# Kernel tuning notes

Measured on AMD Instinct MI355X. Metric: run time of the kernel, lower is better.

## Reference

```python
import jax, jax.numpy as jnp
import numpy as np

B, T, HOR, N = 64, 12, 12, 1024
DIN, DOUT, YCOV, H, K, E = 1, 1, 1, 64, 3, 8


def setup_inputs() -> dict:
    key = jax.random.key(0)
    ks = jax.random.split(key, 10)
    def g(k, shape, s=1.0):
        return jax.random.normal(k, shape, dtype=jnp.float32) * s
    # xavier-ish scale for GCN weights: 1/sqrt(fan_in)
    gi = 1.0 / np.sqrt(K * (DIN + H))
    di = 1.0 / np.sqrt(K * (DOUT + YCOV + H))
    return {
        "x": jax.random.uniform(ks[0], (B, T, N, DIN), dtype=jnp.float32),
        "y_cov": jax.random.uniform(ks[1], (B, HOR, N, YCOV), dtype=jnp.float32),
        "node_emb": g(ks[2], (N, E), 1.0),
        "enc_gate_W": g(ks[3], (K * (DIN + H), 2 * H), gi),
        "enc_gate_b": jnp.zeros((2 * H,), jnp.float32),
        "enc_upd_W": g(ks[4], (K * (DIN + H), H), gi),
        "enc_upd_b": jnp.zeros((H,), jnp.float32),
        "dec_gate_W": g(ks[5], (K * (DOUT + YCOV + H), 2 * H), di),
        "dec_gate_b": jnp.zeros((2 * H,), jnp.float32),
        "dec_upd_W": g(ks[6], (K * (DOUT + YCOV + H), H), di),
        "dec_upd_b": jnp.zeros((H,), jnp.float32),
        "proj_W": g(ks[7], (H, DOUT), 1.0 / np.sqrt(H)),
        "proj_b": jnp.zeros((DOUT,), jnp.float32),
    }


def _cheb_supports(A):
    # support_set = [I, A, 2*A@A - I, ...], cheb_k terms
    s = [jnp.eye(A.shape[0], dtype=A.dtype), A]
    for _ in range(2, K):
        s.append(2.0 * A @ s[-1] - s[-2])
    return jnp.stack(s)  # [K, N, N]


def _gcn(x, sup, W, b):
    # x: [B,N,C]; sup: [K,N,N]; matches torch cat([s_k @ x], -1) ordering (k-major)
    bb, nn, cc = x.shape
    xg = jnp.einsum('knm,bmc->bnkc', sup, x).reshape(bb, nn, K * cc)
    return xg @ W + b


def _cell(x, h, sup, gW, gb, uW, ub):
    zr = jax.nn.sigmoid(_gcn(jnp.concatenate([x, h], -1), sup, gW, gb))
    z, r = jnp.split(zr, 2, axis=-1)
    hc = jnp.tanh(_gcn(jnp.concatenate([x, z * h], -1), sup, uW, ub))
    return r * h + (1.0 - r) * hc


def reference(x, y_cov, node_emb, enc_gate_W, enc_gate_b, enc_upd_W, enc_upd_b,
              dec_gate_W, dec_gate_b, dec_upd_W, dec_upd_b, proj_W, proj_b):
    # adaptive adjacency from node embeddings (AGCRN-style)
    A = jax.nn.softmax(jax.nn.relu(node_emb @ node_emb.T), axis=-1)
    sup = _cheb_supports(A)

    h0 = jnp.zeros((B, N, H), x.dtype)

    def enc_step(h, xt):
        h2 = _cell(xt, h, sup, enc_gate_W, enc_gate_b, enc_upd_W, enc_upd_b)
        return h2, None
    h_enc, _ = jax.lax.scan(enc_step, h0, jnp.swapaxes(x, 0, 1))  # final state [B,N,H]

    go0 = jnp.zeros((B, N, DOUT), x.dtype)

    def dec_step(carry, yt):
        h, go = carry
        h2 = _cell(jnp.concatenate([go, yt], -1), h, sup,
                   dec_gate_W, dec_gate_b, dec_upd_W, dec_upd_b)
        go2 = h2 @ proj_W + proj_b
        return (h2, go2), go2
    _, outs = jax.lax.scan(dec_step, (h_enc, go0), jnp.swapaxes(y_cov, 0, 1))
    return jnp.swapaxes(outs, 0, 1)  # [B, HOR, N, DOUT]
```

## Files before the change

kernel.cpp:

```cpp
#include <hip/hip_runtime.h>
#include <math.h>

constexpr int N = 1024, B = 64, T = 12, HOR = 12, H = 64, E = 8;
constexpr size_t NBH = 4194304;

constexpr size_t A_off   = 0;
constexpr size_t Pxy_off = 1048576;
constexpr size_t h_off   = Pxy_off + 3145728;
constexpr size_t Ph_off  = h_off + NBH;
constexpr size_t zh_off  = Ph_off + 2 * NBH;
constexpr size_t r_off   = zh_off + NBH;
constexpr size_t go_off  = r_off + NBH;
constexpr size_t A2_off  = go_off + 65536;
constexpr size_t Bth_off = A2_off + 1048576;
constexpr size_t Btz_off = Bth_off + 2162688;
constexpr size_t xyK_off = Btz_off + 2097152;
constexpr size_t Pgo_off = xyK_off + 786432;
constexpr size_t wp_off  = Pgo_off + 131072;

typedef __attribute__((ext_vector_type(8))) short short8;
typedef _Float16 half8 __attribute__((ext_vector_type(8)));
typedef __attribute__((ext_vector_type(4))) float f32x4;

__device__ __forceinline__ unsigned f2bf(float x) {
  unsigned u = __float_as_uint(x);
  return (u + 0x7fffu + ((u >> 16) & 1u)) >> 16;
}
__device__ __forceinline__ float bf2f(unsigned h) {
  return __uint_as_float(h << 16);
}
__device__ __forceinline__ ushort f2h(float x) {
  _Float16 h = (_Float16)x;
  ushort u;
  __builtin_memcpy(&u, &h, 2);
  return u;
}
__device__ __forceinline__ void split4(float4 v, uint2& hi, uint2& lo) {
  unsigned h0 = f2bf(v.x), h1 = f2bf(v.y), h2 = f2bf(v.z), h3 = f2bf(v.w);
  unsigned l0 = f2bf(v.x - bf2f(h0)), l1 = f2bf(v.y - bf2f(h1));
  unsigned l2 = f2bf(v.z - bf2f(h2)), l3 = f2bf(v.w - bf2f(h3));
  hi.x = (h0 & 0xffffu) | (h1 << 16); hi.y = (h2 & 0xffffu) | (h3 << 16);
  lo.x = (l0 & 0xffffu) | (l1 << 16); lo.y = (l2 & 0xffffu) | (l3 << 16);
}

typedef const __attribute__((address_space(1))) void gas_t;
typedef __attribute__((address_space(3))) void las_t;

__global__ __launch_bounds__(256) void build_A(const float* __restrict__ emb,
                                               float* __restrict__ A) {
  __shared__ float sE[N * E];
  __shared__ float sv[N];
  __shared__ float rmax[4], rsum[4];
  const int i = blockIdx.x;
  for (int idx = threadIdx.x; idx < N * E / 4; idx += 256)
    ((float4*)sE)[idx] = ((const float4*)emb)[idx];
  __syncthreads();
  float ei[E];
#pragma unroll
  for (int e = 0; e < E; ++e) ei[e] = sE[i * E + e];
  float mymax = 0.f;
  for (int j = threadIdx.x; j < N; j += 256) {
    float d = 0.f;
#pragma unroll
    for (int e = 0; e < E; ++e) d = fmaf(ei[e], sE[j * E + e], d);
    d = fmaxf(d, 0.f);
    sv[j] = d;
    mymax = fmaxf(mymax, d);
  }
  for (int off = 32; off; off >>= 1) mymax = fmaxf(mymax, __shfl_down(mymax, off));
  const int wid = threadIdx.x >> 6, lid = threadIdx.x & 63;
  if (lid == 0) rmax[wid] = mymax;
  __syncthreads();
  const float m = fmaxf(fmaxf(rmax[0], rmax[1]), fmaxf(rmax[2], rmax[3]));
  float mysum = 0.f;
  for (int j = threadIdx.x; j < N; j += 256) {
    float ev = expf(sv[j] - m);
    sv[j] = ev;
    mysum += ev;
  }
  for (int off = 32; off; off >>= 1) mysum += __shfl_down(mysum, off);
  if (lid == 0) rsum[wid] = mysum;
  __syncthreads();
  const float inv = 1.f / (rsum[0] + rsum[1] + rsum[2] + rsum[3]);
  for (int j = threadIdx.x; j < N; j += 256) A[i * N + j] = sv[j] * inv;
}

__global__ __launch_bounds__(256) void pack_split_S(const float* __restrict__ A,
                                                    ushort* __restrict__ L,
                                                    ushort* __restrict__ R) {
  __shared__ float tile[32][33];
  const int bx = blockIdx.x * 32;
  const int by = blockIdx.y * 32;
  const int tx = threadIdx.x & 31;
  const int tg = threadIdx.x >> 5;
#pragma unroll
  for (int p = 0; p < 4; ++p) {
    int ty = tg * 4 + p;
    tile[ty][tx] = A[(size_t)(by + ty) * 1024 + bx + tx];
  }
  __syncthreads();
#pragma unroll
  for (int p = 0; p < 4; ++p) {
    int ty = tg * 4 + p;
    float v = tile[ty][tx];
    unsigned h = f2bf(v);
    unsigned l = f2bf(v - bf2f(h));
    size_t lb = (size_t)(by + ty) * 3072 + 3 * (bx + tx);
    L[lb + 0] = (ushort)h; L[lb + 1] = (ushort)l; L[lb + 2] = (ushort)h;
    float w = tile[tx][ty];
    unsigned hh = f2bf(w);
    unsigned ll = f2bf(w - bf2f(hh));
    size_t rbi = (size_t)(bx + ty) * 3072 + 3 * (by + tx);
    R[rbi + 0] = (ushort)hh; R[rbi + 1] = (ushort)hh; R[rbi + 2] = (ushort)ll;
  }
}

__global__ __launch_bounds__(256) void conv_bf16(const float* __restrict__ src,
                                                 ushort* __restrict__ dst) {
  int i = blockIdx.x * 256 + threadIdx.x;
  float4 v = ((const float4*)src)[i];
  ushort4 o;
  o.x = (ushort)f2bf(v.x); o.y = (ushort)f2bf(v.y);
  o.z = (ushort)f2bf(v.z); o.w = (ushort)f2bf(v.w);
  ((ushort4*)dst)[i] = o;
}

__global__ __launch_bounds__(256) void conv_xyK(const float* __restrict__ src,
                                                ushort* __restrict__ dst, int off) {
  int id = blockIdx.x * 256 + threadIdx.x;
  int tb = id >> 10, n = id & 1023;
  int tt = tb >> 6, b = tb & 63;
  dst[(size_t)(off + tb) * 1024 + n] = (ushort)f2bf(src[((size_t)b * T + tt) * 1024 + n]);
}

__global__ __launch_bounds__(256) void pack_Wbf(const float* __restrict__ W,
                                                ushort* __restrict__ out,
                                                int CIN, int NC, int xoff) {
  int idx = blockIdx.x * 256 + threadIdx.x;
  int total = 2 * NC * 32;
  if (idx >= total) return;
  int kk = idx & 31;
  int rest = idx >> 5;
  int col = rest % NC;
  int half = rest / NC;
  float v = W[(size_t)(xoff + half * 32 + kk) * NC + col];
  unsigned hi = f2bf(v);
  unsigned lo = f2bf(v - bf2f(hi));
  size_t base = (size_t)(half * 2) * NC * 32;
  out[base + (size_t)col * 32 + kk] = (ushort)hi;
  out[base + (size_t)NC * 32 + (size_t)col * 32 + kk] = (ushort)lo;
}

__global__ __launch_bounds__(256) void pack_W16(const float* __restrict__ W,
                                                ushort* __restrict__ out,
                                                int CIN, int NC, int xoff) {
  int idx = blockIdx.x * 256 + threadIdx.x;
  int total = 2 * 2 * NC * 32;
  if (idx >= total) return;
  int kk = idx & 31;
  int rest = idx >> 5;
  int col = rest % NC;
  rest /= NC;
  int half = rest & 1;
  int s1 = rest >> 1;
  int s = s1 + 1;
  float v = W[(size_t)(s * CIN + xoff + half * 32 + kk) * NC + col];
  out[(size_t)(s1 * 2 + half) * NC * 32 + (size_t)col * 32 + kk] = f2h(v);
}

__global__ __launch_bounds__(256) void gemm_s2p(
    const ushort* __restrict__ L, const ushort* __restrict__ R,
    float* __restrict__ P) {
  __shared__ ushort As[128 * 32];
  __shared__ ushort Bs[128 * 32];
  const int t = threadIdx.x;
  const int wave = t >> 6, lane = t & 63;
  const int bm = blockIdx.y * 128, bn = blockIdx.x * 128;
  const int wm = (wave & 1) * 64, wn = (wave >> 1) * 64;
  float* Pz = P + (size_t)blockIdx.z * 1048576;
  const int kbase = blockIdx.z * 768;

  const ushort* aSrc[2]; const ushort* bSrc[2];
  ushort* aDst[2]; ushort* bDst[2];
#pragma unroll
  for (int u = 0; u < 2; ++u) {
    int idx = wave * 128 + u * 64 + lane;
    int row = idx >> 2;
    int kq = (idx & 3) * 8;
    aSrc[u] = L + (size_t)(bm + row) * 3072 + kq;
    bSrc[u] = R + (size_t)(bn + row) * 3072 + kq;
    aDst[u] = &As[(wave * 128 + u * 64) * 8];
    bDst[u] = &Bs[(wave * 128 + u * 64) * 8];
  }
  const int lr = lane & 15;
  const int lk = (lane >> 4) * 8;
  f32x4 acc[4][4];
#pragma unroll
  for (int i = 0; i < 4; ++i)
#pragma unroll
    for (int j = 0; j < 4; ++j) acc[i][j] = {0.f, 0.f, 0.f, 0.f};

  for (int k0 = kbase; k0 < kbase + 768; k0 += 32) {
#pragma unroll
    for (int u = 0; u < 2; ++u) {
      __builtin_amdgcn_global_load_lds((gas_t*)(aSrc[u] + k0), (las_t*)aDst[u], 16, 0, 0);
      __builtin_amdgcn_global_load_lds((gas_t*)(bSrc[u] + k0), (las_t*)bDst[u], 16, 0, 0);
    }
    __syncthreads();
    short8 a[4], b[4];
#pragma unroll
    for (int i = 0; i < 4; ++i) a[i] = *(const short8*)&As[(wm + i * 16 + lr) * 32 + lk];
#pragma unroll
    for (int j = 0; j < 4; ++j) b[j] = *(const short8*)&Bs[(wn + j * 16 + lr) * 32 + lk];
#pragma unroll
    for (int i = 0; i < 4; ++i)
#pragma unroll
      for (int j = 0; j < 4; ++j)
        acc[i][j] = __builtin_amdgcn_mfma_f32_16x16x32_bf16(a[i], b[j], acc[i][j], 0, 0, 0);
    __syncthreads();
  }
  const int cr = (lane >> 4) * 4;
  const int cc = lane & 15;
#pragma unroll
  for (int i = 0; i < 4; ++i)
#pragma unroll
    for (int j = 0; j < 4; ++j) {
      int gm = bm + wm + i * 16 + cr;
      int gn = bn + wn + j * 16 + cc;
#pragma unroll
      for (int r = 0; r < 4; ++r)
        Pz[(size_t)(gm + r) * 1024 + gn] = acc[i][j][r];
    }
}

__global__ __launch_bounds__(256) void comb_s2(const float* __restrict__ P,
                                               ushort* __restrict__ A2) {
  int idx = blockIdx.x * 256 + threadIdx.x;
  float4 a = ((const float4*)P)[idx];
  float4 b = ((const float4*)(P + 1048576))[idx];
  float4 c = ((const float4*)(P + 2097152))[idx];
  float4 d = ((const float4*)(P + 3145728))[idx];
  int base = idx << 2;
  int m = base >> 10, c0 = base & 1023;
  float v0 = 2.f * (a.x + b.x + c.x + d.x) - (m == c0 + 0 ? 1.f : 0.f);
  float v1 = 2.f * (a.y + b.y + c.y + d.y) - (m == c0 + 1 ? 1.f : 0.f);
  float v2 = 2.f * (a.z + b.z + c.z + d.z) - (m == c0 + 2 ? 1.f : 0.f);
  float v3 = 2.f * (a.w + b.w + c.w + d.w) - (m == c0 + 3 ? 1.f : 0.f);
  ushort4 o;
  o.x = (ushort)f2bf(v0); o.y = (ushort)f2bf(v1);
  o.z = (ushort)f2bf(v2); o.w = (ushort)f2bf(v3);
  ((ushort4*)(A2 + 1048576))[idx] = o;
}

template <int CMODE>
__global__ __launch_bounds__(256) void gemm_bt(
    const ushort* __restrict__ A2, const ushort* __restrict__ Bt, int n1,
    ushort* __restrict__ C1h, float* __restrict__ C1f, float* __restrict__ C2) {
  __shared__ ushort As[2][128 * 32];
  __shared__ ushort Bs[2][128 * 32];
  const int t = threadIdx.x;
  const int wave = t >> 6, lane = t & 63;
  int bxi, byi;
  if (CMODE == 0) {
    bxi = blockIdx.x; byi = blockIdx.y;
  } else {
    int lin = blockIdx.x;
    if (lin < 512) {
      bxi = (lin & 7) * 4 + ((lin >> 3) & 3);
      byi = lin >> 5;
    } else {
      bxi = 32; byi = lin - 512;
    }
  }
  const int bm = byi * 128, bn = bxi * 128;
  const int wm = (wave & 1) * 64, wn = (wave >> 1) * 64;

  const ushort* aSrc[2]; const ushort* bSrc[2];
  ushort* aDst[2][2]; ushort* bDst[2][2];
#pragma unroll
  for (int u = 0; u < 2; ++u) {
    int idx = wave * 128 + u * 64 + lane;
    int row = idx >> 2;
    int kq = (idx & 3) * 8;
    aSrc[u] = A2 + (size_t)(bm + row) * 1024 + kq;
    bSrc[u] = Bt + (size_t)(bn + row) * 1024 + kq;
#pragma unroll
    for (int p = 0; p < 2; ++p) {
      aDst[p][u] = &As[p][(wave * 128 + u * 64) * 8];
      bDst[p][u] = &Bs[p][(wave * 128 + u * 64) * 8];
    }
  }
  const int lr = lane & 15, lk = (lane >> 4) * 8;
  int aOff[4], bOff[4];
#pragma unroll
  for (int i = 0; i < 4; ++i) {
    aOff[i] = (wm + i * 16 + lr) * 32 + lk;
    bOff[i] = (wn + i * 16 + lr) * 32 + lk;
  }
  f32x4 acc[4][4];
#pragma unroll
  for (int i = 0; i < 4; ++i)
#pragma unroll
    for (int j = 0; j < 4; ++j) acc[i][j] = {0.f, 0.f, 0.f, 0.f};

  for (int k0 = 0; k0 < 1024; k0 += 64) {
#pragma unroll
    for (int p = 0; p < 2; ++p)
#pragma unroll
      for (int u = 0; u < 2; ++u) {
        __builtin_amdgcn_global_load_lds((gas_t*)(aSrc[u] + k0 + p * 32),
                                         (las_t*)aDst[p][u], 16, 0, 0);
        __builtin_amdgcn_global_load_lds((gas_t*)(bSrc[u] + k0 + p * 32),
                                         (las_t*)bDst[p][u], 16, 0, 0);
      }
    __syncthreads();
#pragma unroll
    for (int p = 0; p < 2; ++p) {
      short8 a[4], b[4];
#pragma unroll
      for (int i = 0; i < 4; ++i) a[i] = *(const short8*)&As[p][aOff[i]];
#pragma unroll
      for (int j = 0; j < 4; ++j) b[j] = *(const short8*)&Bs[p][bOff[j]];
#pragma unroll
      for (int i = 0; i < 4; ++i)
#pragma unroll
        for (int j = 0; j < 4; ++j)
          acc[i][j] = __builtin_amdgcn_mfma_f32_16x16x32_bf16(a[i], b[j], acc[i][j], 0, 0, 0);
    }
    __syncthreads();
  }

  const int cr = (lane >> 4) * 4;
  const int cc = lane & 15;
#pragma unroll
  for (int i = 0; i < 4; ++i) {
#pragma unroll
    for (int j = 0; j < 4; ++j) {
      int gm = bm + wm + i * 16 + cr;
      int gn = bn + wn + j * 16 + cc;
      if (gn < n1) {
        if (CMODE == 0) {
          float* p = C1f + (size_t)gm * n1 + gn;
#pragma unroll
          for (int r = 0; r < 4; ++r) p[(size_t)r * n1] = acc[i][j][r];
        } else {
          int half = gm >> 10, nn = gm & 1023;
          ushort* p = C1h + (size_t)half * NBH +
                      ((size_t)(gn >> 6) * 1024 + nn) * 64 + (gn & 63);
#pragma unroll
          for (int r = 0; r < 4; ++r) p[(size_t)r * 64] = f2h(acc[i][j][r]);
        }
      } else if (C2 != nullptr && gn < n1 + 64) {
        float* p = C2 + (size_t)gm * 64 + (gn - n1);
#pragma unroll
        for (int r = 0; r < 4; ++r) p[(size_t)r * 64] = acc[i][j][r];
      }
    }
  }
}

template <int NX>
__global__ __launch_bounds__(256, 4) void gate_mfma(
    const float* __restrict__ hmat, const ushort* __restrict__ Ph16,
    const ushort* __restrict__ Wbf, const ushort* __restrict__ W16,
    const float* __restrict__ Wf, const float* __restrict__ bias,
    const float* __restrict__ xb0, int xbs0, const float* __restrict__ xp0, int xs0,
    const float* __restrict__ xb1, int xbs1, const float* __restrict__ xp1, int xs1,
    float* __restrict__ zh, float* __restrict__ rbuf, ushort* __restrict__ Btz) {
  constexpr int CIN = NX + 64;
  __shared__ ushort smem[12288];
  ushort* Ah = smem;
  ushort* Al = smem + 2048;
  ushort* Bh = smem + 4096;
  ushort* Bl = smem + 8192;
  ushort* A16 = smem;
  ushort* B16 = smem + 4096;
  ushort* transT = smem;
  __shared__ float sxv[3][2][64];
  __shared__ float sWx[3][2][128];
  const int t = threadIdx.x;
  const int wave = t >> 6, lane = t & 63;
  const int bm = blockIdx.x * 64;
  const int wm = (wave & 1) * 32, wn = (wave >> 1) * 64;
  const int lr = lane & 15, lk = (lane >> 4) * 8;

  if (t < 64) {
    int grow = bm + t;
    int n = grow & 1023, b = grow >> 10;
    sxv[0][0][t] = xb0[(size_t)b * xbs0 + n];
    sxv[1][0][t] = xp0[(size_t)n * xs0 + b];
    sxv[2][0][t] = xp0[(size_t)1024 * xs0 + (size_t)n * xs0 + b];
    if (NX == 2) {
      sxv[0][1][t] = xb1[(size_t)b * xbs1 + n];
      sxv[1][1][t] = xp1[(size_t)n * xs1 + b];
      sxv[2][1][t] = xp1[(size_t)1024 * xs1 + (size_t)n * xs1 + b];
    }
  } else if (t < 192) {
    int col = t - 64;
#pragma unroll
    for (int s = 0; s < 3; ++s)
#pragma unroll
      for (int f = 0; f < NX; ++f)
        sWx[s][f][col] = Wf[(size_t)(s * CIN + f) * 128 + col];
  }

  int arow[2], ajq[2];
#pragma unroll
  for (int p = 0; p < 2; ++p) {
    int f = p * 256 + t;
    arow[p] = f >> 3;
    ajq[p] = (f & 7) * 4;
  }
  const int hrow = t >> 2, hjq = (t & 3) * 8;

  float4 pf[2];
#pragma unroll
  for (int p = 0; p < 2; ++p)
    pf[p] = *(const float4*)(hmat + (size_t)(bm + arow[p]) * 64 + ajq[p]);
  uint4 px;

  f32x4 acc[2][4];
#pragma unroll
  for (int i = 0; i < 2; ++i)
#pragma unroll
    for (int j = 0; j < 4; ++j) acc[i][j] = {0.f, 0.f, 0.f, 0.f};

#pragma unroll
  for (int half = 0; half < 2; ++half) {
#pragma unroll
    for (int p = 0; p < 2; ++p) {
      uint2 hi, lo;
      split4(pf[p], hi, lo);
      *(uint2*)&Ah[arow[p] * 32 + ajq[p]] = hi;
      *(uint2*)&Al[arow[p] * 32 + ajq[p]] = lo;
    }
    const ushort* wph = Wbf + (size_t)(half * 2) * (128 * 32);
    const ushort* wpl = wph + 128 * 32;
#pragma unroll
    for (int u = 0; u < 2; ++u) {
      int idx = wave * 128 + u * 64 + lane;
      __builtin_amdgcn_global_load_lds((gas_t*)(wph + idx * 8), (las_t*)&Bh[idx * 8], 16, 0, 0);
      __builtin_amdgcn_global_load_lds((gas_t*)(wpl + idx * 8), (las_t*)&Bl[idx * 8], 16, 0, 0);
    }
    __syncthreads();
    if (half == 0) {
#pragma unroll
      for (int p = 0; p < 2; ++p)
        pf[p] = *(const float4*)(hmat + (size_t)(bm + arow[p]) * 64 + 32 + ajq[p]);
    } else {
      px = *(const uint4*)(Ph16 + (size_t)(bm + hrow) * 64 + hjq);
    }
    short8 ah[2], al[2], bh[4], bl[4];
#pragma unroll
    for (int i = 0; i < 2; ++i) {
      ah[i] = *(const short8*)&Ah[(wm + i * 16 + lr) * 32 + lk];
      al[i] = *(const short8*)&Al[(wm + i * 16 + lr) * 32 + lk];
    }
#pragma unroll
    for (int j = 0; j < 4; ++j) {
      bh[j] = *(const short8*)&Bh[(wn + j * 16 + lr) * 32 + lk];
      bl[j] = *(const short8*)&Bl[(wn + j * 16 + lr) * 32 + lk];
    }
#pragma unroll
    for (int i = 0; i < 2; ++i)
#pragma unroll
      for (int j = 0; j < 4; ++j) {
        acc[i][j] = __builtin_amdgcn_mfma_f32_16x16x32_bf16(ah[i], bh[j], acc[i][j], 0, 0, 0);
        acc[i][j] = __builtin_amdgcn_mfma_f32_16x16x32_bf16(al[i], bh[j], acc[i][j], 0, 0, 0);
        acc[i][j] = __builtin_amdgcn_mfma_f32_16x16x32_bf16(ah[i], bl[j], acc[i][j], 0, 0, 0);
      }
    __syncthreads();
  }

  for (int it = 0; it < 4; ++it) {
    const int s1 = it >> 1, half = it & 1;
    *(uint4*)&A16[hrow * 32 + hjq] = px;
    const ushort* w16 = W16 + (size_t)(s1 * 2 + half) * (128 * 32);
#pragma unroll
    for (int u = 0; u < 2; ++u) {
      int idx = wave * 128 + u * 64 + lane;
      __builtin_amdgcn_global_load_lds((gas_t*)(w16 + idx * 8), (las_t*)&B16[idx * 8], 16, 0, 0);
    }
    __syncthreads();
    if (it < 3) {
      const int nit = it + 1;
      const ushort* src = Ph16 + (size_t)(nit >> 1) * NBH;
      px = *(const uint4*)(src + (size_t)(bm + hrow) * 64 + (nit & 1) * 32 + hjq);
    }
    half8 a16[2], b16[4];
#pragma unroll
    for (int i = 0; i < 2; ++i)
      a16[i] = *(const half8*)&A16[(wm + i * 16 + lr) * 32 + lk];
#pragma unroll
    for (int j = 0; j < 4; ++j)
      b16[j] = *(const half8*)&B16[(wn + j * 16 + lr) * 32 + lk];
#pragma unroll
    for (int i = 0; i < 2; ++i)
#pragma unroll
      for (int j = 0; j < 4; ++j)
        acc[i][j] = __builtin_amdgcn_mfma_f32_16x16x32_f16(a16[i], b16[j], acc[i][j], 0, 0, 0);
    __syncthreads();
  }

  const int cr = (lane >> 4) * 4;
  const int cc = lane & 15;
#pragma unroll
  for (int i = 0; i < 2; ++i) {
#pragma unroll
    for (int j = 0; j < 4; ++j) {
      int col = wn + j * 16 + cc;
      float bcol = bias[col];
#pragma unroll
      for (int r = 0; r < 4; ++r) {
        int rowl = wm + i * 16 + cr + r;
        int grow = bm + rowl;
        float v = acc[i][j][r] + bcol;
#pragma unroll
        for (int s = 0; s < 3; ++s)
#pragma unroll
          for (int f = 0; f < NX; ++f)
            v = fmaf(sxv[s][f][rowl], sWx[s][f][col], v);
        float sig = 1.f / (1.f + expf(-v));
        if (col < 64) {
          float zv = sig * hmat[(size_t)grow * 64 + col];
          zh[(size_t)grow * 64 + col] = zv;
          transT[col * 72 + rowl] = (ushort)f2bf(zv);
        } else {
          rbuf[(size_t)grow * 64 + col - 64] = sig;
        }
      }
    }
  }
  __syncthreads();
  const int bq = bm >> 10, nb = bm & 1023;
  for (int idx = t; idx < 512; idx += 256) {
    int j = idx >> 3, ch = idx & 7;
    uint4 v = *(const uint4*)&transT[j * 72 + ch * 8];
    *(uint4*)(Btz + (((size_t)(bq * 64 + j)) << 10) + nb + ch * 8) = v;
  }
}

template <int NX, int PROJ>
__global__ __launch_bounds__(256, 4) void upd_mfma(
    float* __restrict__ hmat, const float* __restrict__ zhb, const ushort* __restrict__ Pzh16,
    const ushort* __restrict__ Wbf, const ushort* __restrict__ W16,
    const float* __restrict__ Wf, const float* __restrict__ bias,
    const float* __restrict__ xb0, int xbs0, const float* __restrict__ xp0, int xs0,
    const float* __restrict__ xb1, int xbs1, const float* __restrict__ xp1, int xs1,
    const float* __restrict__ rbuf, ushort* __restrict__ Bth,
    const float* __restrict__ pW, const float* __restrict__ pb,
    float* __restrict__ gobuf, float* __restrict__ outp, int tstep) {
  constexpr int CIN = NX + 64;
  __shared__ ushort smem[8192];
  ushort* Ah = smem;
  ushort* Al = smem + 2048;
  ushort* Bh = smem + 4096;
  ushort* Bl = smem + 6144;
  ushort* A16 = smem;
  ushort* B16 = smem + 4096;
  ushort* transT = smem;
  __shared__ float sxv[3][2][64];
  __shared__ float sWx[3][2][64];
  __shared__ float part[2][64];
  const int t = threadIdx.x;
  const int wave = t >> 6, lane = t & 63;
  const int bm = blockIdx.x * 64;
  const int wm = (wave & 1) * 32, wn = (wave >> 1) * 32;
  const int lr = lane & 15, lk = (lane >> 4) * 8;

  if (t < 64) {
    int grow = bm + t;
    int n = grow & 1023, b = grow >> 10;
    sxv[0][0][t] = xb0[(size_t)b * xbs0 + n];
    sxv[1][0][t] = xp0[(size_t)n * xs0 + b];
    sxv[2][0][t] = xp0[(size_t)1024 * xs0 + (size_t)n * xs0 + b];
    if (NX == 2) {
      sxv[0][1][t] = xb1[(size_t)b * xbs1 + n];
      sxv[1][1][t] = xp1[(size_t)n * xs1 + b];
      sxv[2][1][t] = xp1[(size_t)1024 * xs1 + (size_t)n * xs1 + b];
    }
  } else if (t < 128) {
    int col = t - 64;
#pragma unroll
    for (int s = 0; s < 3; ++s)
#pragma unroll
      for (int f = 0; f < NX; ++f)
        sWx[s][f][col] = Wf[(size_t)(s * CIN + f) * 64 + col];
  }

  int arow[2], ajq[2];
#pragma unroll
  for (int p = 0; p < 2; ++p) {
    int f = p * 256 + t;
    arow[p] = f >> 3;
    ajq[p] = (f & 7) * 4;
  }
  const int hrow = t >> 2, hjq = (t & 3) * 8;

  float4 pf[2];
#pragma unroll
  for (int p = 0; p < 2; ++p)
    pf[p] = *(const float4*)(zhb + (size_t)(bm + arow[p]) * 64 + ajq[p]);
  uint4 px;

  f32x4 acc[2][2];
#pragma unroll
  for (int i = 0; i < 2; ++i)
#pragma unroll
    for (int j = 0; j < 2; ++j) acc[i][j] = {0.f, 0.f, 0.f, 0.f};

#pragma unroll
  for (int half = 0; half < 2; ++half) {
#pragma unroll
    for (int p = 0; p < 2; ++p) {
      uint2 hi, lo;
      split4(pf[p], hi, lo);
      *(uint2*)&Ah[arow[p] * 32 + ajq[p]] = hi;
      *(uint2*)&Al[arow[p] * 32 + ajq[p]] = lo;
    }
    const ushort* wph = Wbf + (size_t)(half * 2) * (64 * 32);
    const ushort* wpl = wph + 64 * 32;
    {
      int idx = wave * 64 + lane;
      __builtin_amdgcn_global_load_lds((gas_t*)(wph + idx * 8), (las_t*)&Bh[idx * 8], 16, 0, 0);
      __builtin_amdgcn_global_load_lds((gas_t*)(wpl + idx * 8), (las_t*)&Bl[idx * 8], 16, 0, 0);
    }
    __syncthreads();
    if (half == 0) {
#pragma unroll
      for (int p = 0; p < 2; ++p)
        pf[p] = *(const float4*)(zhb + (size_t)(bm + arow[p]) * 64 + 32 + ajq[p]);
    } else {
      px = *(const uint4*)(Pzh16 + (size_t)(bm + hrow) * 64 + hjq);
    }
    short8 ah[2], al[2], bh[2], bl[2];
#pragma unroll
    for (int i = 0; i < 2; ++i) {
      ah[i] = *(const short8*)&Ah[(wm + i * 16 + lr) * 32 + lk];
      al[i] = *(const short8*)&Al[(wm + i * 16 + lr) * 32 + lk];
    }
#pragma unroll
    for (int j = 0; j < 2; ++j) {
      bh[j] = *(const short8*)&Bh[(wn + j * 16 + lr) * 32 + lk];
      bl[j] = *(const short8*)&Bl[(wn + j * 16 + lr) * 32 + lk];
    }
#pragma unroll
    for (int i = 0; i < 2; ++i)
#pragma unroll
      for (int j = 0; j < 2; ++j) {
        acc[i][j] = __builtin_amdgcn_mfma_f32_16x16x32_bf16(ah[i], bh[j], acc[i][j], 0, 0, 0);
        acc[i][j] = __builtin_amdgcn_mfma_f32_16x16x32_bf16(al[i], bh[j], acc[i][j], 0, 0, 0);
        acc[i][j] = __builtin_amdgcn_mfma_f32_16x16x32_bf16(ah[i], bl[j], acc[i][j], 0, 0, 0);
      }
    __syncthreads();
  }

  for (int it = 0; it < 4; ++it) {
    const int s1 = it >> 1, half = it & 1;
    *(uint4*)&A16[hrow * 32 + hjq] = px;
    const ushort* w16 = W16 + (size_t)(s1 * 2 + half) * (64 * 32);
    {
      int idx = wave * 64 + lane;
      __builtin_amdgcn_global_load_lds((gas_t*)(w16 + idx * 8), (las_t*)&B16[idx * 8], 16, 0, 0);
    }
    __syncthreads();
    if (it < 3) {
      const int nit = it + 1;
      const ushort* src = Pzh16 + (size_t)(nit >> 1) * NBH;
      px = *(const uint4*)(src + (size_t)(bm + hrow) * 64 + (nit & 1) * 32 + hjq);
    }
    half8 a16[2], b16[2];
#pragma unroll
    for (int i = 0; i < 2; ++i)
      a16[i] = *(const half8*)&A16[(wm + i * 16 + lr) * 32 + lk];
#pragma unroll
    for (int j = 0; j < 2; ++j)
      b16[j] = *(const half8*)&B16[(wn + j * 16 + lr) * 32 + lk];
#pragma unroll
    for (int i = 0; i < 2; ++i)
#pragma unroll
      for (int j = 0; j < 2; ++j)
        acc[i][j] = __builtin_amdgcn_mfma_f32_16x16x32_f16(a16[i], b16[j], acc[i][j], 0, 0, 0);
    __syncthreads();
  }

  const int cr = (lane >> 4) * 4;
  const int cc = lane & 15;
  float psv[2][4];
#pragma unroll
  for (int i = 0; i < 2; ++i)
#pragma unroll
    for (int r = 0; r < 4; ++r) psv[i][r] = 0.f;

#pragma unroll
  for (int i = 0; i < 2; ++i) {
#pragma unroll
    for (int j = 0; j < 2; ++j) {
      int col = wn + j * 16 + cc;
      float bcol = bias[col];
      float pwc = PROJ ? pW[col] : 0.f;
#pragma unroll
      for (int r = 0; r < 4; ++r) {
        int rowl = wm + i * 16 + cr + r;
        int grow = bm + rowl;
        float v = acc[i][j][r] + bcol;
#pragma unroll
        for (int s = 0; s < 3; ++s)
#pragma unroll
          for (int f = 0; f < NX; ++f)
            v = fmaf(sxv[s][f][rowl], sWx[s][f][col], v);
        float hc = tanhf(v);
        size_t idx = (size_t)grow * 64 + col;
        float rr = rbuf[idx];
        float ho = hmat[idx];
        float o = rr * ho + (1.f - rr) * hc;
        hmat[idx] = o;
        transT[col * 72 + rowl] = (ushort)f2bf(o);
        if (PROJ) psv[i][r] += o * pwc;
      }
    }
  }
  if (PROJ) {
#pragma unroll
    for (int i = 0; i < 2; ++i)
#pragma unroll
      for (int r = 0; r < 4; ++r)
#pragma unroll
        for (int off = 8; off; off >>= 1)
          psv[i][r] += __shfl_down(psv[i][r], off, 16);
    if (cc == 0) {
#pragma unroll
      for (int i = 0; i < 2; ++i)
#pragma unroll
        for (int r = 0; r < 4; ++r)
          part[wn >> 5][wm + i * 16 + cr + r] = psv[i][r];
    }
  }
  __syncthreads();
  const int bq = bm >> 10, nb = bm & 1023;
  for (int idx = t; idx < 512; idx += 256) {
    int j = idx >> 3, ch = idx & 7;
    uint4 v = *(const uint4*)&transT[j * 72 + ch * 8];
    *(uint4*)(Bth + (((size_t)(bq * 64 + j)) << 10) + nb + ch * 8) = v;
  }
  if (PROJ && t < 64) {
    int grow = bm + t;
    int n = grow & 1023, b = grow >> 10;
    float g = part[0][t] + part[1][t] + pb[0];
    gobuf[grow] = g;
    outp[((size_t)b * HOR + tstep) * N + n] = g;
    Bth[((size_t)(4096 + b)) * 1024 + n] = (ushort)f2bf(g);
  }
}

extern "C" void kernel_launch(void* const* d_in, const int* in_sizes, int n_in,
                              void* d_out, int out_size, void* d_ws, size_t ws_size,
                              hipStream_t stream) {
  const float* x    = (const float*)d_in[0];
  const float* ycov = (const float*)d_in[1];
  const float* emb  = (const float*)d_in[2];
  const float* egW  = (const float*)d_in[3];
  const float* egb  = (const float*)d_in[4];
  const float* euW  = (const float*)d_in[5];
  const float* eub  = (const float*)d_in[6];
  const float* dgW  = (const float*)d_in[7];
  const float* dgb  = (const float*)d_in[8];
  const float* duW  = (const float*)d_in[9];
  const float* dub  = (const float*)d_in[10];
  const float* pW   = (const float*)d_in[11];
  const float* pb   = (const float*)d_in[12];
  float* out = (float*)d_out;
  float* ws  = (float*)d_ws;

  float* Amat = ws + A_off;
  float* Pxy  = ws + Pxy_off;
  float* hmat = ws + h_off;
  ushort* Ph16 = (ushort*)(ws + Ph_off);
  float* zh   = ws + zh_off;
  float* rb   = ws + r_off;
  float* gob  = ws + go_off;
  float* Pgo  = ws + Pgo_off;
  ushort* A2   = (ushort*)(ws + A2_off);
  ushort* Bth  = (ushort*)(ws + Bth_off);
  ushort* Btz  = (ushort*)(ws + Btz_off);
  ushort* xyK  = (ushort*)(ws + xyK_off);
  ushort* AspL = (ushort*)(ws + zh_off);
  ushort* AspR = (ushort*)(ws + r_off);
  float*  Pp   = ws + Ph_off;
  ushort* WB   = (ushort*)(ws + wp_off);
  ushort* WbfGE = WB;
  ushort* WbfGD = WB + 16384;
  ushort* WbfUE = WB + 32768;
  ushort* WbfUD = WB + 40960;
  ushort* W16GE = WB + 49152;
  ushort* W16GD = WB + 65536;
  ushort* W16UE = WB + 81920;
  ushort* W16UD = WB + 90112;

  build_A<<<N, 256, 0, stream>>>(emb, Amat);
  pack_split_S<<<dim3(32, 32), 256, 0, stream>>>(Amat, AspL, AspR);
  gemm_s2p<<<dim3(8, 8, 4), 256, 0, stream>>>(AspL, AspR, Pp);
  comb_s2<<<1024, 256, 0, stream>>>(Pp, A2);
  conv_bf16<<<1024, 256, 0, stream>>>(Amat, A2);
  conv_xyK<<<3072, 256, 0, stream>>>(x, xyK, 0);
  conv_xyK<<<3072, 256, 0, stream>>>(ycov, xyK, 768);
  pack_Wbf<<<32, 256, 0, stream>>>(egW, WbfGE, 65, 128, 1);
  pack_Wbf<<<32, 256, 0, stream>>>(dgW, WbfGD, 66, 128, 2);
  pack_Wbf<<<16, 256, 0, stream>>>(euW, WbfUE, 65, 64, 1);
  pack_Wbf<<<16, 256, 0, stream>>>(duW, WbfUD, 66, 64, 2);
  pack_W16<<<64, 256, 0, stream>>>(egW, W16GE, 65, 128, 1);
  pack_W16<<<64, 256, 0, stream>>>(dgW, W16GD, 66, 128, 2);
  pack_W16<<<32, 256, 0, stream>>>(euW, W16UE, 65, 64, 1);
  pack_W16<<<32, 256, 0, stream>>>(duW, W16UD, 66, 64, 2);
  gemm_bt<0><<<dim3(12, 16), 256, 0, stream>>>(A2, xyK, 1536, nullptr, Pxy, nullptr);
  (void)hipMemsetAsync(hmat, 0, NBH * sizeof(float), stream);
  (void)hipMemsetAsync(Ph16, 0, 2 * NBH * sizeof(ushort), stream);
  (void)hipMemsetAsync(gob, 0, 65536 * sizeof(float), stream);
  (void)hipMemsetAsync(Bth + (size_t)4096 * 1024, 0, 128 * 1024 * sizeof(ushort), stream);

  for (int t = 0; t < T; ++t) {
    if (t > 0)
      gemm_bt<1><<<512, 256, 0, stream>>>(A2, Bth, 4096, Ph16, nullptr, nullptr);
    gate_mfma<1><<<1024, 256, 0, stream>>>(hmat, Ph16, WbfGE, W16GE, egW, egb,
                                           x + t * 1024, T * 1024, Pxy + t * 64, 1536,
                                           nullptr, 0, nullptr, 0, zh, rb, Btz);
    if (t > 0)
      gemm_bt<1><<<512, 256, 0, stream>>>(A2, Btz, 4096, Ph16, nullptr, nullptr);
    upd_mfma<1, 0><<<1024, 256, 0, stream>>>(hmat, zh, Ph16, WbfUE, W16UE, euW, eub,
                                             x + t * 1024, T * 1024, Pxy + t * 64, 1536,
                                             nullptr, 0, nullptr, 0, rb, Bth,
                                             nullptr, nullptr, nullptr, nullptr, 0);
  }

  for (int t = 0; t < HOR; ++t) {
    gemm_bt<1><<<528, 256, 0, stream>>>(A2, Bth, 4096, Ph16, nullptr, Pgo);
    gate_mfma<2><<<1024, 256, 0, stream>>>(hmat, Ph16, WbfGD, W16GD, dgW, dgb,
                                           gob, 1024, Pgo, 64,
                                           ycov + t * 1024, HOR * 1024,
                                           Pxy + 768 + t * 64, 1536, zh, rb, Btz);
    gemm_bt<1><<<512, 256, 0, stream>>>(A2, Btz, 4096, Ph16, nullptr, nullptr);
    upd_mfma<2, 1><<<1024, 256, 0, stream>>>(hmat, zh, Ph16, WbfUD, W16UD, duW, dub,
                                             gob, 1024, Pgo, 64,
                                             ycov + t * 1024, HOR * 1024,
                                             Pxy + 768 + t * 64, 1536,
                                             rb, Bth, pW, pb, gob, out, t);
  }
}
```

Measured before the change: 2.504 ms.

## Split the adjacency GEMM along K into two halves summed by consumers

The recurrent gemm_bt now launches twice as many blocks. Each block covers half of the 1024-long K dimension and writes its fp16 partial result to one of two buffers. The gate and update kernels load both partials and add them in fp16 before the MFMA stage. This gives better CU occupancy on the 512-block grid, which was below what the GPU can hold at once. In exchange the fp16 traffic written and read doubles, and there is an extra fp16 rounding step.

```diff
diff --git a/kernel.cpp b/kernel.cpp
--- a/kernel.cpp
+++ b/kernel.cpp
@@ -17,6 +17,7 @@
 constexpr size_t xyK_off = Btz_off + 2097152;
 constexpr size_t Pgo_off = xyK_off + 786432;
 constexpr size_t wp_off  = Pgo_off + 131072;
+constexpr size_t Phb_off = wp_off + 49152;
 
 typedef __attribute__((ext_vector_type(8))) short short8;
 typedef _Float16 half8 __attribute__((ext_vector_type(8)));
@@ -255,25 +256,29 @@
 template <int CMODE>
 __global__ __launch_bounds__(256) void gemm_bt(
     const ushort* __restrict__ A2, const ushort* __restrict__ Bt, int n1,
-    ushort* __restrict__ C1h, float* __restrict__ C1f, float* __restrict__ C2) {
+    ushort* __restrict__ C1h, ushort* __restrict__ C1hB,
+    float* __restrict__ C1f, float* __restrict__ C2) {
   __shared__ ushort As[2][128 * 32];
   __shared__ ushort Bs[2][128 * 32];
   const int t = threadIdx.x;
   const int wave = t >> 6, lane = t & 63;
-  int bxi, byi;
+  int bxi, byi, z;
   if (CMODE == 0) {
-    bxi = blockIdx.x; byi = blockIdx.y;
+    bxi = blockIdx.x; byi = blockIdx.y; z = 2;
   } else {
     int lin = blockIdx.x;
-    if (lin < 512) {
+    if (lin < 1024) {
+      z = lin >> 9;
       bxi = (lin & 7) * 4 + ((lin >> 3) & 3);
-      byi = lin >> 5;
+      byi = (lin >> 5) & 15;
     } else {
-      bxi = 32; byi = lin - 512;
+      z = 2; bxi = 32; byi = lin - 1024;
     }
   }
   const int bm = byi * 128, bn = bxi * 128;
   const int wm = (wave & 1) * 64, wn = (wave >> 1) * 64;
+  const int kbeg = (z == 1) ? 512 : 0;
+  const int kend = (z == 0) ? 512 : 1024;
 
   const ushort* aSrc[2]; const ushort* bSrc[2];
   ushort* aDst[2][2]; ushort* bDst[2][2];
@@ -303,7 +308,7 @@
 #pragma unroll
     for (int j = 0; j < 4; ++j) acc[i][j] = {0.f, 0.f, 0.f, 0.f};
 
-  for (int k0 = 0; k0 < 1024; k0 += 64) {
+  for (int k0 = kbeg; k0 < kend; k0 += 64) {
 #pragma unroll
     for (int p = 0; p < 2; ++p)
 #pragma unroll
@@ -332,6 +337,7 @@
 
   const int cr = (lane >> 4) * 4;
   const int cc = lane & 15;
+  ushort* C1dst = (z == 1) ? C1hB : C1h;
 #pragma unroll
   for (int i = 0; i < 4; ++i) {
 #pragma unroll
@@ -345,7 +351,7 @@
           for (int r = 0; r < 4; ++r) p[(size_t)r * n1] = acc[i][j][r];
         } else {
           int half = gm >> 10, nn = gm & 1023;
-          ushort* p = C1h + (size_t)half * NBH +
+          ushort* p = C1dst + (size_t)half * NBH +
                       ((size_t)(gn >> 6) * 1024 + nn) * 64 + (gn & 63);
 #pragma unroll
           for (int r = 0; r < 4; ++r) p[(size_t)r * 64] = f2h(acc[i][j][r]);
@@ -362,6 +368,7 @@
 template <int NX>
 __global__ __launch_bounds__(256, 4) void gate_mfma(
     const float* __restrict__ hmat, const ushort* __restrict__ Ph16,
+    const ushort* __restrict__ Ph16b,
     const ushort* __restrict__ Wbf, const ushort* __restrict__ W16,
     const float* __restrict__ Wf, const float* __restrict__ bias,
     const float* __restrict__ xb0, int xbs0, const float* __restrict__ xp0, int xs0,
@@ -417,7 +424,7 @@
 #pragma unroll
   for (int p = 0; p < 2; ++p)
     pf[p] = *(const float4*)(hmat + (size_t)(bm + arow[p]) * 64 + ajq[p]);
-  uint4 px;
+  uint4 px0, px1;
 
   f32x4 acc[2][4];
 #pragma unroll
@@ -448,7 +455,9 @@
       for (int p = 0; p < 2; ++p)
         pf[p] = *(const float4*)(hmat + (size_t)(bm + arow[p]) * 64 + 32 + ajq[p]);
     } else {
-      px = *(const uint4*)(Ph16 + (size_t)(bm + hrow) * 64 + hjq);
+      size_t off0 = (size_t)(bm + hrow) * 64 + hjq;
+      px0 = *(const uint4*)(Ph16 + off0);
+      px1 = *(const uint4*)(Ph16b + off0);
     }
     short8 ah[2], al[2], bh[4], bl[4];
 #pragma unroll
@@ -474,7 +483,13 @@
 
   for (int it = 0; it < 4; ++it) {
     const int s1 = it >> 1, half = it & 1;
-    *(uint4*)&A16[hrow * 32 + hjq] = px;
+    {
+      half8 h0, h1;
+      __builtin_memcpy(&h0, &px0, 16);
+      __builtin_memcpy(&h1, &px1, 16);
+      half8 hs = h0 + h1;
+      *(half8*)&A16[hrow * 32 + hjq] = hs;
+    }
     const ushort* w16 = W16 + (size_t)(s1 * 2 + half) * (128 * 32);
 #pragma unroll
     for (int u = 0; u < 2; ++u) {
@@ -484,8 +499,9 @@
     __syncthreads();
     if (it < 3) {
       const int nit = it + 1;
-      const ushort* src = Ph16 + (size_t)(nit >> 1) * NBH;
-      px = *(const uint4*)(src + (size_t)(bm + hrow) * 64 + (nit & 1) * 32 + hjq);
+      size_t off = (size_t)(nit >> 1) * NBH + (size_t)(bm + hrow) * 64 + (nit & 1) * 32 + hjq;
+      px0 = *(const uint4*)(Ph16 + off);
+      px1 = *(const uint4*)(Ph16b + off);
     }
     half8 a16[2], b16[4];
 #pragma unroll
@@ -542,7 +558,8 @@
 
 template <int NX, int PROJ>
 __global__ __launch_bounds__(256, 4) void upd_mfma(
-    float* __restrict__ hmat, const float* __restrict__ zhb, const ushort* __restrict__ Pzh16,
+    float* __restrict__ hmat, const float* __restrict__ zhb,
+    const ushort* __restrict__ Pzh16, const ushort* __restrict__ Pzh16b,
     const ushort* __restrict__ Wbf, const ushort* __restrict__ W16,
     const float* __restrict__ Wf, const float* __restrict__ bias,
     const float* __restrict__ xb0, int xbs0, const float* __restrict__ xp0, int xs0,
@@ -601,7 +618,7 @@
 #pragma unroll
   for (int p = 0; p < 2; ++p)
     pf[p] = *(const float4*)(zhb + (size_t)(bm + arow[p]) * 64 + ajq[p]);
-  uint4 px;
+  uint4 px0, px1;
 
   f32x4 acc[2][2];
 #pragma unroll
@@ -631,7 +648,9 @@
       for (int p = 0; p < 2; ++p)
         pf[p] = *(const float4*)(zhb + (size_t)(bm + arow[p]) * 64 + 32 + ajq[p]);
     } else {
-      px = *(const uint4*)(Pzh16 + (size_t)(bm + hrow) * 64 + hjq);
+      size_t off0 = (size_t)(bm + hrow) * 64 + hjq;
+      px0 = *(const uint4*)(Pzh16 + off0);
+      px1 = *(const uint4*)(Pzh16b + off0);
     }
     short8 ah[2], al[2], bh[2], bl[2];
 #pragma unroll
@@ -657,7 +676,13 @@
 
   for (int it = 0; it < 4; ++it) {
     const int s1 = it >> 1, half = it & 1;
-    *(uint4*)&A16[hrow * 32 + hjq] = px;
+    {
+      half8 h0, h1;
+      __builtin_memcpy(&h0, &px0, 16);
+      __builtin_memcpy(&h1, &px1, 16);
+      half8 hs = h0 + h1;
+      *(half8*)&A16[hrow * 32 + hjq] = hs;
+    }
     const ushort* w16 = W16 + (size_t)(s1 * 2 + half) * (64 * 32);
     {
       int idx = wave * 64 + lane;
@@ -666,8 +691,9 @@
     __syncthreads();
     if (it < 3) {
       const int nit = it + 1;
-      const ushort* src = Pzh16 + (size_t)(nit >> 1) * NBH;
-      px = *(const uint4*)(src + (size_t)(bm + hrow) * 64 + (nit & 1) * 32 + hjq);
+      size_t off = (size_t)(nit >> 1) * NBH + (size_t)(bm + hrow) * 64 + (nit & 1) * 32 + hjq;
+      px0 = *(const uint4*)(Pzh16 + off);
+      px1 = *(const uint4*)(Pzh16b + off);
     }
     half8 a16[2], b16[2];
 #pragma unroll
@@ -775,7 +801,8 @@
   float* Amat = ws + A_off;
   float* Pxy  = ws + Pxy_off;
   float* hmat = ws + h_off;
-  ushort* Ph16 = (ushort*)(ws + Ph_off);
+  ushort* Ph16  = (ushort*)(ws + Ph_off);
+  ushort* Ph16b = (ushort*)(ws + Phb_off);
   float* zh   = ws + zh_off;
   float* rb   = ws + r_off;
   float* gob  = ws + go_off;
@@ -812,34 +839,35 @@
   pack_W16<<<64, 256, 0, stream>>>(dgW, W16GD, 66, 128, 2);
   pack_W16<<<32, 256, 0, stream>>>(euW, W16UE, 65, 64, 1);
   pack_W16<<<32, 256, 0, stream>>>(duW, W16UD, 66, 64, 2);
-  gemm_bt<0><<<dim3(12, 16), 256, 0, stream>>>(A2, xyK, 1536, nullptr, Pxy, nullptr);
+  gemm_bt<0><<<dim3(12, 16), 256, 0, stream>>>(A2, xyK, 1536, nullptr, nullptr, Pxy, nullptr);
   (void)hipMemsetAsync(hmat, 0, NBH * sizeof(float), stream);
   (void)hipMemsetAsync(Ph16, 0, 2 * NBH * sizeof(ushort), stream);
+  (void)hipMemsetAsync(Ph16b, 0, 2 * NBH * sizeof(ushort), stream);
   (void)hipMemsetAsync(gob, 0, 65536 * sizeof(float), stream);
   (void)hipMemsetAsync(Bth + (size_t)4096 * 1024, 0, 128 * 1024 * sizeof(ushort), stream);
 
   for (int t = 0; t < T; ++t) {
     if (t > 0)
-      gemm_bt<1><<<512, 256, 0, stream>>>(A2, Bth, 4096, Ph16, nullptr, nullptr);
-    gate_mfma<1><<<1024, 256, 0, stream>>>(hmat, Ph16, WbfGE, W16GE, egW, egb,
+      gemm_bt<1><<<1024, 256, 0, stream>>>(A2, Bth, 4096, Ph16, Ph16b, nullptr, nullptr);
+    gate_mfma<1><<<1024, 256, 0, stream>>>(hmat, Ph16, Ph16b, WbfGE, W16GE, egW, egb,
                                            x + t * 1024, T * 1024, Pxy + t * 64, 1536,
                                            nullptr, 0, nullptr, 0, zh, rb, Btz);
     if (t > 0)
-      gemm_bt<1><<<512, 256, 0, stream>>>(A2, Btz, 4096, Ph16, nullptr, nullptr);
-    upd_mfma<1, 0><<<1024, 256, 0, stream>>>(hmat, zh, Ph16, WbfUE, W16UE, euW, eub,
+      gemm_bt<1><<<1024, 256, 0, stream>>>(A2, Btz, 4096, Ph16, Ph16b, nullptr, nullptr);
+    upd_mfma<1, 0><<<1024, 256, 0, stream>>>(hmat, zh, Ph16, Ph16b, WbfUE, W16UE, euW, eub,
                                              x + t * 1024, T * 1024, Pxy + t * 64, 1536,
                                              nullptr, 0, nullptr, 0, rb, Bth,
                                              nullptr, nullptr, nullptr, nullptr, 0);
   }
 
   for (int t = 0; t < HOR; ++t) {
-    gemm_bt<1><<<528, 256, 0, stream>>>(A2, Bth, 4096, Ph16, nullptr, Pgo);
-    gate_mfma<2><<<1024, 256, 0, stream>>>(hmat, Ph16, WbfGD, W16GD, dgW, dgb,
+    gemm_bt<1><<<1040, 256, 0, stream>>>(A2, Bth, 4096, Ph16, Ph16b, nullptr, Pgo);
+    gate_mfma<2><<<1024, 256, 0, stream>>>(hmat, Ph16, Ph16b, WbfGD, W16GD, dgW, dgb,
                                            gob, 1024, Pgo, 64,
                                            ycov + t * 1024, HOR * 1024,
                                            Pxy + 768 + t * 64, 1536, zh, rb, Btz);
-    gemm_bt<1><<<512, 256, 0, stream>>>(A2, Btz, 4096, Ph16, nullptr, nullptr);
-    upd_mfma<2, 1><<<1024, 256, 0, stream>>>(hmat, zh, Ph16, WbfUD, W16UD, duW, dub,
+    gemm_bt<1><<<1024, 256, 0, stream>>>(A2, Btz, 4096, Ph16, Ph16b, nullptr, nullptr);
+    upd_mfma<2, 1><<<1024, 256, 0, stream>>>(hmat, zh, Ph16, Ph16b, WbfUD, W16UD, duW, dub,
                                              gob, 1024, Pgo, 64,
                                              ycov + t * 1024, HOR * 1024,
                                              Pxy + 768 + t * 64, 1536,
```

Measured after the change: 2.890 ms. 1.15x slower.
